# Performance work log

Hardware: AMD Instinct MI355X
Metric: run time of the kernel (lower is better)

## Reference

```python
import jax, jax.numpy as jnp
import numpy as np
import math

N_EMBD = 1024
N_HEAD = 16
BLOCK = 2048
SPARSITY = 0.25
B, T = 2, 2048


def _make_mask_logits(rng):
    # Replicates the patterned init in SparseMixtureAttention.__init__.
    S = BLOCK
    logits = np.empty((N_HEAD, S, S), dtype=np.float32)
    for h in range(N_HEAD):
        if h % 3 == 0:  # banded pattern (bandwidth 16)
            i = np.arange(S)
            band = (np.abs(i[:, None] - i[None, :]) <= 16)
            logits[h] = np.where(band, rng.standard_normal((S, S)) + 2.0,
                                 rng.standard_normal((S, S)) - 2.0)
        elif h % 3 == 1:  # strided pattern: every 4th column
            strided = (np.arange(S)[None, :] % 4 == 0)
            logits[h] = np.where(strided, rng.standard_normal((S, S)) + 2.0,
                                 rng.standard_normal((S, S)) - 2.0)
        else:  # random pattern with given sparsity
            rnd = rng.random((S, S)) < SPARSITY
            logits[h] = np.where(rnd, rng.standard_normal((S, S)) + 2.0,
                                 rng.standard_normal((S, S)) - 2.0)
    # keep the diagonal unmasked so no causal row is fully masked (avoids NaN rows)
    d = np.arange(S)
    logits[:, d, d] = np.abs(logits[:, d, d]) + 2.0
    return logits.astype(np.float32)


def setup_inputs() -> dict:
    key = jax.random.key(0)
    ks = jax.random.split(key, 5)
    rng = np.random.default_rng(0)
    return {
        "x": jax.random.normal(ks[0], (B, T, N_EMBD), dtype=jnp.float32),
        "mask_logits": jnp.asarray(_make_mask_logits(rng)),
        "W_attn": jax.random.normal(ks[1], (3 * N_EMBD, N_EMBD), dtype=jnp.float32) * 0.02,
        "b_attn": jnp.zeros((3 * N_EMBD,), dtype=jnp.float32),
        "W_proj": jax.random.normal(ks[2], (N_EMBD, N_EMBD), dtype=jnp.float32) * 0.02,
        "b_proj": jnp.zeros((N_EMBD,), dtype=jnp.float32),
    }


def reference(x, mask_logits, W_attn, b_attn, W_proj, b_proj):
    Bx, Tx, C = x.shape
    H = mask_logits.shape[0]
    D = C // H
    qkv = x @ W_attn.T + b_attn                       # [B,T,3C]
    q, k, v = jnp.split(qkv, 3, axis=-1)
    q = q.reshape(Bx, Tx, H, D)
    k = k.reshape(Bx, Tx, H, D)
    v = v.reshape(Bx, Tx, H, D)
    att = jnp.einsum('bthd,bshd->bhts', q, k) * (1.0 / math.sqrt(D))  # [B,H,T,T]
    # forward value of the STE mask equals the hard mask (probs - probs.detach() == 0)
    keep = jax.nn.sigmoid(mask_logits[:, :Tx, :Tx]) > 0.5             # [H,T,T]
    causal = jnp.tril(jnp.ones((Tx, Tx), dtype=bool))
    mask = causal[None, :, :] & keep                                  # [H,T,T]
    att = jnp.where(mask[None], att, -jnp.inf)
    att = jax.nn.softmax(att, axis=-1)
    y = jnp.einsum('bhts,bshd->bthd', att, v).reshape(Bx, Tx, C)
    return y @ W_proj.T + b_proj
```

## Files before the change

### kernel.cpp

```cpp
#include <hip/hip_runtime.h>
#include <hip/hip_bf16.h>
#include <stdint.h>

typedef unsigned short u16;
typedef unsigned int u32;
typedef unsigned long long u64;
typedef __attribute__((ext_vector_type(8))) short bf16x8;
typedef __attribute__((ext_vector_type(4))) float f32x4;
typedef __attribute__((ext_vector_type(4))) u32 u32x4;

#define NB 2
#define NH 16
#define TT 2048
#define DD 64
#define CC 1024

__device__ __forceinline__ u16 bf16bits(float f) {
    __hip_bfloat16 h = __float2bfloat16(f);
    return __builtin_bit_cast(unsigned short, h);
}

__device__ __forceinline__ void gload_lds16(const void* g, void* l) {
    __builtin_amdgcn_global_load_lds(
        (const __attribute__((address_space(1))) void*)g,
        (__attribute__((address_space(3))) void*)l, 16, 0, 0);
}

__global__ __launch_bounds__(256) void prep_all(
    const float* __restrict__ x, const float* __restrict__ Wa_f,
    const float* __restrict__ Wp_f, const float* __restrict__ ml,
    u16* __restrict__ xb, u16* __restrict__ wab, u16* __restrict__ wpb,
    unsigned char* __restrict__ mb) {
    const int bid = blockIdx.x;
    if (bid < 512) {
        int idx = bid * 256 + threadIdx.x;
        for (int i = idx; i < 2097152; i += 512 * 256) {
            const float* src; u16* dst; int off;
            if (i < 1048576)      { src = x;    dst = xb;  off = i; }
            else if (i < 1835008) { src = Wa_f; dst = wab; off = i - 1048576; }
            else                  { src = Wp_f; dst = wpb; off = i - 1835008; }
            float4 v = reinterpret_cast<const float4*>(src)[off];
            ushort4 o;
            o.x = bf16bits(v.x); o.y = bf16bits(v.y);
            o.z = bf16bits(v.z); o.w = bf16bits(v.w);
            reinterpret_cast<ushort4*>(dst)[off] = o;
        }
    } else {
        const int wid = ((bid - 512) << 2) + (threadIdx.x >> 6);
        const int lane = threadIdx.x & 63;
        const int i0 = wid & 2047;
        const int hbase = (wid >> 11) << 3;
#pragma unroll 1
        for (int k = 0; k < 8; ++k) {
            int h = hbase + k;
            int i = (k & 1) ? (2047 - i0) : i0;
            int row = h * 2048 + i;
            const float* src = ml + (size_t)row * TT;
            unsigned char* dst = mb + (size_t)row * (TT / 8);
#pragma unroll 1
            for (int c8 = lane; c8 < 256; c8 += 64) {
                unsigned char v = 0;
                if (c8 * 8 <= i) {
                    const float4* p = reinterpret_cast<const float4*>(src + c8 * 8);
                    float4 a = p[0];
                    float4 b = p[1];
                    unsigned u = 0;
                    u |= (a.x > 0.f) ? 1u : 0u;
                    u |= (a.y > 0.f) ? 2u : 0u;
                    u |= (a.z > 0.f) ? 4u : 0u;
                    u |= (a.w > 0.f) ? 8u : 0u;
                    u |= (b.x > 0.f) ? 16u : 0u;
                    u |= (b.y > 0.f) ? 32u : 0u;
                    u |= (b.z > 0.f) ? 64u : 0u;
                    u |= (b.w > 0.f) ? 128u : 0u;
                    int rem = i - c8 * 8;
                    if (rem < 7) u &= (1u << (rem + 1)) - 1;
                    v = (unsigned char)u;
                }
                dst[c8] = v;
            }
        }
    }
}

__global__ __launch_bounds__(256) void gemm_qkv(
    const u16* __restrict__ A, const u16* __restrict__ Bw,
    const float* __restrict__ bias,
    u16* __restrict__ Qb, u16* __restrict__ Kb, u16* __restrict__ Vtb) {
    const int bm = blockIdx.y * 128;
    const int bn = blockIdx.x * 128;
    const int tid = threadIdx.x;
    const int w = tid >> 6, lane = tid & 63;
    const int lrow = lane & 15, lgrp = lane >> 4;
    const int wr = (w >> 1) * 64, wc = (w & 1) * 64;

    __shared__ __align__(16) u16 ABs[2][128 * 64];
    u16* As = ABs[0];
    u16* Bs = ABs[1];

    f32x4 acc[4][4] = {};

    for (int kt = 0; kt < 16; ++kt) {
        const int k0 = kt << 6;
#pragma unroll
        for (int i = 0; i < 4; ++i) {
            int e = i * 2048 + tid * 8;
            int r = e >> 6, c = e & 63;
            gload_lds16(A + (size_t)(bm + r) * CC + k0 + c, (char*)As + i * 4096 + w * 1024);
            gload_lds16(Bw + (size_t)(bn + r) * CC + k0 + c, (char*)Bs + i * 4096 + w * 1024);
        }
        __syncthreads();
#pragma unroll
        for (int kk = 0; kk < 2; ++kk) {
            bf16x8 af[4], bfz[4];
#pragma unroll
            for (int i = 0; i < 4; ++i)
                af[i] = *reinterpret_cast<const bf16x8*>(&As[(wr + i * 16 + lrow) * 64 + kk * 32 + lgrp * 8]);
#pragma unroll
            for (int i = 0; i < 4; ++i)
                bfz[i] = *reinterpret_cast<const bf16x8*>(&Bs[(wc + i * 16 + lrow) * 64 + kk * 32 + lgrp * 8]);
#pragma unroll
            for (int mi = 0; mi < 4; ++mi)
#pragma unroll
                for (int ni = 0; ni < 4; ++ni)
                    acc[mi][ni] = __builtin_amdgcn_mfma_f32_16x16x32_bf16(af[mi], bfz[ni], acc[mi][ni], 0, 0, 0);
        }
        __syncthreads();
    }

    const int sec = bn >> 10;

    if (sec == 2) {
        u16* Tl = &ABs[0][0];
#pragma unroll
        for (int ni = 0; ni < 4; ++ni) {
            int nl = wc + ni * 16 + lrow;
            float bv = bias[bn + nl];
#pragma unroll
            for (int mi = 0; mi < 4; ++mi) {
                int ml2 = wr + mi * 16 + lgrp * 4;
                u64 pk = 0;
#pragma unroll
                for (int j = 0; j < 4; ++j)
                    pk |= (u64)bf16bits(acc[mi][ni][j] + bv) << (16 * j);
                int byte = nl * 256 + ((ml2 * 2) ^ ((nl & 7) << 4));
                *reinterpret_cast<u64*>((char*)Tl + byte) = pk;
            }
        }
        __syncthreads();
        int r = tid >> 1, half = tid & 1;
        int h = ((bn & 1023) >> 6) + (r >> 6);
        int d = r & 63;
        int b = bm >> 11;
        u16* gdst = Vtb + (((size_t)b * NH + h) * DD + d) * TT + (bm & 2047) + half * 64;
#pragma unroll
        for (int c = 0; c < 8; ++c) {
            uint4 v = *reinterpret_cast<const uint4*>(
                (char*)Tl + r * 256 + ((half * 128 + c * 16) ^ ((r & 7) << 4)));
            *reinterpret_cast<uint4*>(gdst + c * 8) = v;
        }
        return;
    }

#pragma unroll
    for (int ni = 0; ni < 4; ++ni) {
        int n = bn + wc + ni * 16 + lrow;
        float bv = bias[n];
#pragma unroll
        for (int mi = 0; mi < 4; ++mi) {
#pragma unroll
            for (int j = 0; j < 4; ++j) {
                int m = bm + wr + mi * 16 + lgrp * 4 + j;
                float v = acc[mi][ni][j] + bv;
                int h = (n & 1023) >> 6;
                int d = n & 63;
                int b = m >> 11;
                int t = m & 2047;
                if (sec == 0) {
                    Qb[(((size_t)b * NH + h) * TT + t) * DD + d] =
                        bf16bits(v * (0.125f * 1.4426950408889634f));
                } else {
                    Kb[(((size_t)b * NH + h) * TT + t) * DD + d] = bf16bits(v);
                }
            }
        }
    }
}

__global__ __launch_bounds__(256) void gemm_proj(
    const u16* __restrict__ A, const u16* __restrict__ Bw,
    const float* __restrict__ bias, float* __restrict__ Cout) {
    const int bm = blockIdx.y * 64;
    const int bn = blockIdx.x * 128;
    const int tid = threadIdx.x;
    const int w = tid >> 6, lane = tid & 63;
    const int lrow = lane & 15, lgrp = lane >> 4;
    const int wr = (w >> 1) * 32, wc = (w & 1) * 64;

    __shared__ __align__(16) u16 As[64 * 64];
    __shared__ __align__(16) u16 Bs[128 * 64];

    f32x4 acc[2][4] = {};

    for (int kt = 0; kt < 16; ++kt) {
        const int k0 = kt << 6;
#pragma unroll
        for (int i = 0; i < 2; ++i) {
            int e = i * 2048 + tid * 8;
            int r = e >> 6, c = e & 63;
            gload_lds16(A + (size_t)(bm + r) * CC + k0 + c, (char*)As + i * 4096 + w * 1024);
        }
#pragma unroll
        for (int i = 0; i < 4; ++i) {
            int e = i * 2048 + tid * 8;
            int r = e >> 6, c = e & 63;
            gload_lds16(Bw + (size_t)(bn + r) * CC + k0 + c, (char*)Bs + i * 4096 + w * 1024);
        }
        __syncthreads();
#pragma unroll
        for (int kk = 0; kk < 2; ++kk) {
            bf16x8 af[2], bfz[4];
#pragma unroll
            for (int i = 0; i < 2; ++i)
                af[i] = *reinterpret_cast<const bf16x8*>(&As[(wr + i * 16 + lrow) * 64 + kk * 32 + lgrp * 8]);
#pragma unroll
            for (int i = 0; i < 4; ++i)
                bfz[i] = *reinterpret_cast<const bf16x8*>(&Bs[(wc + i * 16 + lrow) * 64 + kk * 32 + lgrp * 8]);
#pragma unroll
            for (int mi = 0; mi < 2; ++mi)
#pragma unroll
                for (int ni = 0; ni < 4; ++ni)
                    acc[mi][ni] = __builtin_amdgcn_mfma_f32_16x16x32_bf16(af[mi], bfz[ni], acc[mi][ni], 0, 0, 0);
        }
        __syncthreads();
    }

#pragma unroll
    for (int ni = 0; ni < 4; ++ni) {
        int n = bn + wc + ni * 16 + lrow;
        float bv = bias[n];
#pragma unroll
        for (int mi = 0; mi < 2; ++mi) {
#pragma unroll
            for (int j = 0; j < 4; ++j) {
                int m = bm + wr + mi * 16 + lgrp * 4 + j;
                Cout[(size_t)m * 1024 + n] = acc[mi][ni][j] + bv;
            }
        }
    }
}

__global__ __launch_bounds__(256) void attn_kernel(
    const u16* __restrict__ Qb, const u16* __restrict__ Kb,
    const u16* __restrict__ Vtb, const unsigned char* __restrict__ mb,
    u16* __restrict__ att_out) {
    const int slot = blockIdx.x >> 4;
    const int h = blockIdx.x & 15;
    const int b = blockIdx.y;
    const int qt = (slot < 16) ? (31 - slot) : (slot - 16);
    const int tid = threadIdx.x;
    const int w = tid >> 6, lane = tid & 63;
    const int lrow = lane & 15, g = lane >> 4;

    __shared__ __align__(16) u16 Ks[2][64 * 64];
    __shared__ __align__(16) u16 Vts[2][64 * 64];

    const u16* kg_base = &Kb[((size_t)b * NH + h) * TT * DD];
    const u16* vg_base = &Vtb[((size_t)b * NH + h) * DD * TT];

    auto STAGE = [&](int bufi, int kt) {
#pragma unroll
        for (int i = 0; i < 2; ++i) {
            int e = i * 2048 + tid * 8;
            int r = e >> 6, c = e & 63;
            int cs = c ^ ((r & 7) << 3);
            gload_lds16(kg_base + (size_t)kt * 64 * DD + r * DD + cs,
                        (char*)Ks[bufi] + i * 4096 + w * 1024);
            gload_lds16(vg_base + kt * 64 + (size_t)r * TT + cs,
                        (char*)Vts[bufi] + i * 4096 + w * 1024);
        }
    };

    const int qrow_g = qt * 64 + w * 16 + lrow;
    const int rswz = (lrow & 7) << 4;

    bf16x8 qf[2];
#pragma unroll
    for (int kk = 0; kk < 2; ++kk)
        qf[kk] = *reinterpret_cast<const bf16x8*>(
            &Qb[(((size_t)b * NH + h) * TT + qrow_g) * DD + kk * 32 + g * 8]);

    f32x4 oacc[4] = {};
    float l_part = 0.f;

    const unsigned char* mrow_base = mb + ((size_t)h * TT + qrow_g) * (TT / 8);

    STAGE(0, 0);
    int buf = 0;

#pragma unroll 1
    for (int kt = 0; kt <= qt; ++kt) {
        u64 mw = *reinterpret_cast<const u64*>(mrow_base + kt * 8);
        asm volatile("s_waitcnt vmcnt(1)" ::: "memory");
        __builtin_amdgcn_sched_barrier(0);
        asm volatile("s_barrier" ::: "memory");
        if (kt < qt) STAGE(buf ^ 1, kt + 1);

        f32x4 s[4] = {};
        __builtin_amdgcn_s_setprio(1);
#pragma unroll
        for (int kk = 0; kk < 2; ++kk)
#pragma unroll
            for (int nt = 0; nt < 4; ++nt) {
                bf16x8 kf = *reinterpret_cast<const bf16x8*>(
                    (char*)Ks[buf] + (((nt * 16 + lrow) * 128 + (kk * 32 + g * 8) * 2) ^ rswz));
                s[nt] = __builtin_amdgcn_mfma_f32_16x16x32_bf16(kf, qf[kk], s[nt], 0, 0, 0);
            }
        __builtin_amdgcn_s_setprio(0);

        u64 mws = mw >> (g * 4);
        u32 wlo = (u32)mws, whi = (u32)(mws >> 32);
#pragma unroll
        for (int nt = 0; nt < 4; ++nt)
#pragma unroll
            for (int j = 0; j < 4; ++j) {
                int bi = nt * 16 + j;
                u32 word = (bi < 32) ? wlo : whi;
                u32 pm = (u32)(((int)(word << (31 - (bi & 31)))) >> 31);
                float p = __builtin_bit_cast(float,
                          __builtin_bit_cast(u32, exp2f(s[nt][j])) & pm);
                l_part += p;
                s[nt][j] = p;
            }

        u32 X[4][2];
#pragma unroll
        for (int nt = 0; nt < 4; ++nt)
#pragma unroll
            for (int t = 0; t < 2; ++t)
                asm("v_cvt_pk_bf16_f32 %0, %1, %2"
                    : "=v"(X[nt][t]) : "v"(s[nt][2 * t]), "v"(s[nt][2 * t + 1]));

        bf16x8 pf[2];
#pragma unroll
        for (int kk = 0; kk < 2; ++kk) {
            u32 pw[4];
#pragma unroll
            for (int t = 0; t < 2; ++t) {
                u32 a = X[2 * kk][t], b2 = X[2 * kk + 1][t];
                asm("v_permlane32_swap_b32 %0, %1" : "+v"(a), "+v"(b2));
                asm("v_permlane16_swap_b32 %0, %1" : "+v"(a), "+v"(b2));
                pw[t] = a;
                pw[t + 2] = b2;
            }
            u32x4 wv = {pw[0], pw[1], pw[2], pw[3]};
            pf[kk] = __builtin_bit_cast(bf16x8, wv);
        }

        __builtin_amdgcn_s_setprio(1);
#pragma unroll
        for (int kk = 0; kk < 2; ++kk)
#pragma unroll
            for (int dt = 0; dt < 4; ++dt) {
                bf16x8 vf = *reinterpret_cast<const bf16x8*>(
                    (char*)Vts[buf] + (((dt * 16 + lrow) * 128 + (kk * 32 + g * 8) * 2) ^ rswz));
                oacc[dt] = __builtin_amdgcn_mfma_f32_16x16x32_bf16(pf[kk], vf, oacc[dt], 0, 0, 0);
            }
        __builtin_amdgcn_s_setprio(0);

        buf ^= 1;
    }

    float l_run = l_part;
    l_run += __shfl_xor(l_run, 16);
    l_run += __shfl_xor(l_run, 32);
    float lb[4];
#pragma unroll
    for (int j = 0; j < 4; ++j)
        lb[j] = __shfl(l_run, (lane & 48) + g * 4 + j);
#pragma unroll
    for (int dt = 0; dt < 4; ++dt)
#pragma unroll
        for (int j = 0; j < 4; ++j) {
            int t = qt * 64 + w * 16 + g * 4 + j;
            float o = oacc[dt][j] / lb[j];
            att_out[((size_t)b * TT + t) * CC + h * DD + dt * 16 + lrow] = bf16bits(o);
        }
}

extern "C" void kernel_launch(void* const* d_in, const int* in_sizes, int n_in,
                              void* d_out, int out_size, void* d_ws, size_t ws_size,
                              hipStream_t stream) {
    const float* x = (const float*)d_in[0];
    const float* mask_logits = (const float*)d_in[1];
    const float* W_attn = (const float*)d_in[2];
    const float* b_attn = (const float*)d_in[3];
    const float* W_proj = (const float*)d_in[4];
    const float* b_proj = (const float*)d_in[5];
    float* out = (float*)d_out;

    char* ws = (char*)d_ws;
    u16* xb  = (u16*)(ws + 0);
    u16* Wa  = (u16*)(ws + (8u << 20));
    u16* Wp  = (u16*)(ws + (14u << 20));
    u16* Qb  = (u16*)(ws + (16u << 20));
    u16* Kb  = (u16*)(ws + (24u << 20));
    u16* Vtb = (u16*)(ws + (32u << 20));
    u16* att = (u16*)(ws + (40u << 20));
    unsigned char* mbits = (unsigned char*)(ws + (48u << 20));

    prep_all<<<1536, 256, 0, stream>>>(x, W_attn, W_proj, mask_logits,
                                       xb, Wa, Wp, mbits);
    gemm_qkv<<<dim3(24, 32), 256, 0, stream>>>(xb, Wa, b_attn, Qb, Kb, Vtb);
    attn_kernel<<<dim3(512, 2), 256, 0, stream>>>(Qb, Kb, Vtb, mbits, att);
    gemm_proj<<<dim3(8, 64), 256, 0, stream>>>(att, Wp, b_proj, out);
}
```

Baseline: 150.4 us.

## Split attention key tiles across wave pairs with two query rows per wave

Restructures the attention kernel's work split. Each wave now handles 32 query rows as two 16-row groups, reusing every K/V fragment read from shared memory across both groups. The two wave pairs alternate key tiles by parity, and their partial outputs and row sums are combined through shared memory at the end. This aims to cut LDS fragment reads per MFMA and to add independent MFMA chains. In exchange it needs more registers, leaves half the waves idle on each tile, and adds a final cross-wave reduction.

```diff
diff --git a/kernel.cpp b/kernel.cpp
--- a/kernel.cpp
+++ b/kernel.cpp
@@ -261,6 +261,8 @@
     const int tid = threadIdx.x;
     const int w = tid >> 6, lane = tid & 63;
     const int lrow = lane & 15, g = lane >> 4;
+    const int pw = w >> 1;
+    const int rh = w & 1;
 
     __shared__ __align__(16) u16 Ks[2][64 * 64];
     __shared__ __align__(16) u16 Vts[2][64 * 64];
@@ -281,110 +283,183 @@
         }
     };
 
-    const int qrow_g = qt * 64 + w * 16 + lrow;
+    const int qr0 = qt * 64 + rh * 32 + lrow;
+    const int qr1 = qr0 + 16;
     const int rswz = (lrow & 7) << 4;
 
-    bf16x8 qf[2];
-#pragma unroll
-    for (int kk = 0; kk < 2; ++kk)
-        qf[kk] = *reinterpret_cast<const bf16x8*>(
-            &Qb[(((size_t)b * NH + h) * TT + qrow_g) * DD + kk * 32 + g * 8]);
-
-    f32x4 oacc[4] = {};
-    float l_part = 0.f;
-
-    const unsigned char* mrow_base = mb + ((size_t)h * TT + qrow_g) * (TT / 8);
+    bf16x8 qf0[2], qf1[2];
+#pragma unroll
+    for (int kk = 0; kk < 2; ++kk) {
+        qf0[kk] = *reinterpret_cast<const bf16x8*>(
+            &Qb[(((size_t)b * NH + h) * TT + qr0) * DD + kk * 32 + g * 8]);
+        qf1[kk] = *reinterpret_cast<const bf16x8*>(
+            &Qb[(((size_t)b * NH + h) * TT + qr1) * DD + kk * 32 + g * 8]);
+    }
+
+    f32x4 oacc0[4] = {}, oacc1[4] = {};
+    float lp0 = 0.f, lp1 = 0.f;
+
+    const unsigned char* mrow0 = mb + ((size_t)h * TT + qr0) * (TT / 8);
+    const unsigned char* mrow1 = mb + ((size_t)h * TT + qr1) * (TT / 8);
 
     STAGE(0, 0);
     int buf = 0;
 
 #pragma unroll 1
     for (int kt = 0; kt <= qt; ++kt) {
-        u64 mw = *reinterpret_cast<const u64*>(mrow_base + kt * 8);
-        asm volatile("s_waitcnt vmcnt(1)" ::: "memory");
+        u64 mw0 = *reinterpret_cast<const u64*>(mrow0 + kt * 8);
+        u64 mw1 = *reinterpret_cast<const u64*>(mrow1 + kt * 8);
+        asm volatile("s_waitcnt vmcnt(2)" ::: "memory");
         __builtin_amdgcn_sched_barrier(0);
         asm volatile("s_barrier" ::: "memory");
         if (kt < qt) STAGE(buf ^ 1, kt + 1);
 
-        f32x4 s[4] = {};
-        __builtin_amdgcn_s_setprio(1);
-#pragma unroll
-        for (int kk = 0; kk < 2; ++kk)
-#pragma unroll
-            for (int nt = 0; nt < 4; ++nt) {
-                bf16x8 kf = *reinterpret_cast<const bf16x8*>(
-                    (char*)Ks[buf] + (((nt * 16 + lrow) * 128 + (kk * 32 + g * 8) * 2) ^ rswz));
-                s[nt] = __builtin_amdgcn_mfma_f32_16x16x32_bf16(kf, qf[kk], s[nt], 0, 0, 0);
-            }
-        __builtin_amdgcn_s_setprio(0);
-
-        u64 mws = mw >> (g * 4);
-        u32 wlo = (u32)mws, whi = (u32)(mws >> 32);
-#pragma unroll
-        for (int nt = 0; nt < 4; ++nt)
-#pragma unroll
-            for (int j = 0; j < 4; ++j) {
-                int bi = nt * 16 + j;
-                u32 word = (bi < 32) ? wlo : whi;
-                u32 pm = (u32)(((int)(word << (31 - (bi & 31)))) >> 31);
-                float p = __builtin_bit_cast(float,
-                          __builtin_bit_cast(u32, exp2f(s[nt][j])) & pm);
-                l_part += p;
-                s[nt][j] = p;
-            }
-
-        u32 X[4][2];
-#pragma unroll
-        for (int nt = 0; nt < 4; ++nt)
-#pragma unroll
-            for (int t = 0; t < 2; ++t)
-                asm("v_cvt_pk_bf16_f32 %0, %1, %2"
-                    : "=v"(X[nt][t]) : "v"(s[nt][2 * t]), "v"(s[nt][2 * t + 1]));
-
-        bf16x8 pf[2];
-#pragma unroll
-        for (int kk = 0; kk < 2; ++kk) {
-            u32 pw[4];
-#pragma unroll
-            for (int t = 0; t < 2; ++t) {
-                u32 a = X[2 * kk][t], b2 = X[2 * kk + 1][t];
-                asm("v_permlane32_swap_b32 %0, %1" : "+v"(a), "+v"(b2));
-                asm("v_permlane16_swap_b32 %0, %1" : "+v"(a), "+v"(b2));
-                pw[t] = a;
-                pw[t + 2] = b2;
-            }
-            u32x4 wv = {pw[0], pw[1], pw[2], pw[3]};
-            pf[kk] = __builtin_bit_cast(bf16x8, wv);
-        }
-
-        __builtin_amdgcn_s_setprio(1);
-#pragma unroll
-        for (int kk = 0; kk < 2; ++kk)
-#pragma unroll
-            for (int dt = 0; dt < 4; ++dt) {
-                bf16x8 vf = *reinterpret_cast<const bf16x8*>(
-                    (char*)Vts[buf] + (((dt * 16 + lrow) * 128 + (kk * 32 + g * 8) * 2) ^ rswz));
-                oacc[dt] = __builtin_amdgcn_mfma_f32_16x16x32_bf16(pf[kk], vf, oacc[dt], 0, 0, 0);
-            }
-        __builtin_amdgcn_s_setprio(0);
+        if ((kt & 1) == pw) {
+            f32x4 s0[4] = {}, s1[4] = {};
+            __builtin_amdgcn_s_setprio(1);
+#pragma unroll
+            for (int kk = 0; kk < 2; ++kk)
+#pragma unroll
+                for (int nt = 0; nt < 4; ++nt) {
+                    bf16x8 kf = *reinterpret_cast<const bf16x8*>(
+                        (char*)Ks[buf] + (((nt * 16 + lrow) * 128 + (kk * 32 + g * 8) * 2) ^ rswz));
+                    s0[nt] = __builtin_amdgcn_mfma_f32_16x16x32_bf16(kf, qf0[kk], s0[nt], 0, 0, 0);
+                    s1[nt] = __builtin_amdgcn_mfma_f32_16x16x32_bf16(kf, qf1[kk], s1[nt], 0, 0, 0);
+                }
+            __builtin_amdgcn_s_setprio(0);
+
+            bf16x8 pf0[2], pf1[2];
+            {
+                u64 mws = mw0 >> (g * 4);
+                u32 wlo = (u32)mws, whi = (u32)(mws >> 32);
+#pragma unroll
+                for (int nt = 0; nt < 4; ++nt)
+#pragma unroll
+                    for (int j = 0; j < 4; ++j) {
+                        int bi = nt * 16 + j;
+                        u32 word = (bi < 32) ? wlo : whi;
+                        u32 pm = (u32)(((int)(word << (31 - (bi & 31)))) >> 31);
+                        float p = __builtin_bit_cast(float,
+                                  __builtin_bit_cast(u32, exp2f(s0[nt][j])) & pm);
+                        lp0 += p;
+                        s0[nt][j] = p;
+                    }
+                u32 X[4][2];
+#pragma unroll
+                for (int nt = 0; nt < 4; ++nt)
+#pragma unroll
+                    for (int t = 0; t < 2; ++t)
+                        asm("v_cvt_pk_bf16_f32 %0, %1, %2"
+                            : "=v"(X[nt][t]) : "v"(s0[nt][2 * t]), "v"(s0[nt][2 * t + 1]));
+#pragma unroll
+                for (int kk = 0; kk < 2; ++kk) {
+                    u32 pwd[4];
+#pragma unroll
+                    for (int t = 0; t < 2; ++t) {
+                        u32 a = X[2 * kk][t], b2 = X[2 * kk + 1][t];
+                        asm("v_permlane32_swap_b32 %0, %1" : "+v"(a), "+v"(b2));
+                        asm("v_permlane16_swap_b32 %0, %1" : "+v"(a), "+v"(b2));
+                        pwd[t] = a;
+                        pwd[t + 2] = b2;
+                    }
+                    u32x4 wv = {pwd[0], pwd[1], pwd[2], pwd[3]};
+                    pf0[kk] = __builtin_bit_cast(bf16x8, wv);
+                }
+            }
+            {
+                u64 mws = mw1 >> (g * 4);
+                u32 wlo = (u32)mws, whi = (u32)(mws >> 32);
+#pragma unroll
+                for (int nt = 0; nt < 4; ++nt)
+#pragma unroll
+                    for (int j = 0; j < 4; ++j) {
+                        int bi = nt * 16 + j;
+                        u32 word = (bi < 32) ? wlo : whi;
+                        u32 pm = (u32)(((int)(word << (31 - (bi & 31)))) >> 31);
+                        float p = __builtin_bit_cast(float,
+                                  __builtin_bit_cast(u32, exp2f(s1[nt][j])) & pm);
+                        lp1 += p;
+                        s1[nt][j] = p;
+                    }
+                u32 X[4][2];
+#pragma unroll
+                for (int nt = 0; nt < 4; ++nt)
+#pragma unroll
+                    for (int t = 0; t < 2; ++t)
+                        asm("v_cvt_pk_bf16_f32 %0, %1, %2"
+                            : "=v"(X[nt][t]) : "v"(s1[nt][2 * t]), "v"(s1[nt][2 * t + 1]));
+#pragma unroll
+                for (int kk = 0; kk < 2; ++kk) {
+                    u32 pwd[4];
+#pragma unroll
+                    for (int t = 0; t < 2; ++t) {
+                        u32 a = X[2 * kk][t], b2 = X[2 * kk + 1][t];
+                        asm("v_permlane32_swap_b32 %0, %1" : "+v"(a), "+v"(b2));
+                        asm("v_permlane16_swap_b32 %0, %1" : "+v"(a), "+v"(b2));
+                        pwd[t] = a;
+                        pwd[t + 2] = b2;
+                    }
+                    u32x4 wv = {pwd[0], pwd[1], pwd[2], pwd[3]};
+                    pf1[kk] = __builtin_bit_cast(bf16x8, wv);
+                }
+            }
+
+            __builtin_amdgcn_s_setprio(1);
+#pragma unroll
+            for (int kk = 0; kk < 2; ++kk)
+#pragma unroll
+                for (int dt = 0; dt < 4; ++dt) {
+                    bf16x8 vf = *reinterpret_cast<const bf16x8*>(
+                        (char*)Vts[buf] + (((dt * 16 + lrow) * 128 + (kk * 32 + g * 8) * 2) ^ rswz));
+                    oacc0[dt] = __builtin_amdgcn_mfma_f32_16x16x32_bf16(pf0[kk], vf, oacc0[dt], 0, 0, 0);
+                    oacc1[dt] = __builtin_amdgcn_mfma_f32_16x16x32_bf16(pf1[kk], vf, oacc1[dt], 0, 0, 0);
+                }
+            __builtin_amdgcn_s_setprio(0);
+        }
 
         buf ^= 1;
     }
 
-    float l_run = l_part;
-    l_run += __shfl_xor(l_run, 16);
-    l_run += __shfl_xor(l_run, 32);
-    float lb[4];
-#pragma unroll
-    for (int j = 0; j < 4; ++j)
-        lb[j] = __shfl(l_run, (lane & 48) + g * 4 + j);
+    __syncthreads();
+    char* cb = (rh == 0) ? (char*)Ks : (char*)Vts;
+    if (pw == 1) {
+#pragma unroll
+        for (int dt = 0; dt < 4; ++dt) {
+            *reinterpret_cast<f32x4*>(cb + lane * 144 + dt * 16) = oacc0[dt];
+            *reinterpret_cast<f32x4*>(cb + lane * 144 + 64 + dt * 16) = oacc1[dt];
+        }
+        *reinterpret_cast<float2*>(cb + lane * 144 + 128) = {lp0, lp1};
+    }
+    __syncthreads();
+    if (pw == 1) return;
+
+#pragma unroll
+    for (int dt = 0; dt < 4; ++dt) {
+        oacc0[dt] += *reinterpret_cast<const f32x4*>(cb + lane * 144 + dt * 16);
+        oacc1[dt] += *reinterpret_cast<const f32x4*>(cb + lane * 144 + 64 + dt * 16);
+    }
+    float2 lp = *reinterpret_cast<const float2*>(cb + lane * 144 + 128);
+    lp0 += lp.x;
+    lp1 += lp.y;
+
+    float l0 = lp0, l1 = lp1;
+    l0 += __shfl_xor(l0, 16); l0 += __shfl_xor(l0, 32);
+    l1 += __shfl_xor(l1, 16); l1 += __shfl_xor(l1, 32);
+    float lb0[4], lb1[4];
+#pragma unroll
+    for (int j = 0; j < 4; ++j) {
+        lb0[j] = __shfl(l0, (lane & 48) + g * 4 + j);
+        lb1[j] = __shfl(l1, (lane & 48) + g * 4 + j);
+    }
 #pragma unroll
     for (int dt = 0; dt < 4; ++dt)
 #pragma unroll
         for (int j = 0; j < 4; ++j) {
-            int t = qt * 64 + w * 16 + g * 4 + j;
-            float o = oacc[dt][j] / lb[j];
-            att_out[((size_t)b * TT + t) * CC + h * DD + dt * 16 + lrow] = bf16bits(o);
+            int t0 = qt * 64 + rh * 32 + g * 4 + j;
+            att_out[((size_t)b * TT + t0) * CC + h * DD + dt * 16 + lrow] =
+                bf16bits(oacc0[dt][j] / lb0[j]);
+            att_out[((size_t)b * TT + t0 + 16) * CC + h * DD + dt * 16 + lrow] =
+                bf16bits(oacc1[dt][j] / lb1[j]);
         }
 }
 
```

Result: slower. 186.3 us (+23.9%).
